# Kernel tuning notes

Hardware: AMD Instinct MI355X
Metric: run time of the kernel (lower is better)

## Reference

```python
import jax, jax.numpy as jnp
import numpy as np

Q_DIM = 9   # state(7) + action(2)
KV_DIM = 5  # fixed by get_input_tensors: 4 relative features + r_trans
H = 3
D = KV_DIM * H  # 15


def setup_inputs() -> dict:
    key = jax.random.key(0)
    ks = jax.random.split(key, 16)
    b, t = 32, 256

    def u(k, shape, fan_in):
        lim = (1.0 / fan_in) ** 0.5
        return jax.random.uniform(k, shape, jnp.float32, -lim, lim)

    return {
        "state": jax.random.normal(ks[0], (b, t, 7), jnp.float32),
        "action": jax.random.normal(ks[1], (b, t, 2), jnp.float32),
        "Wk": u(ks[2], (D, KV_DIM), KV_DIM),
        "Wq": u(ks[3], (D, Q_DIM), Q_DIM),
        "Wv": u(ks[4], (D, KV_DIM), KV_DIM),
        "att_bias": jax.random.uniform(ks[5], (KV_DIM,), jnp.float32, -0.1, 0.1),
        "Wscore": u(ks[6], (1, KV_DIM), KV_DIM),
        "bscore": u(ks[7], (1,), KV_DIM),
        "g1": jnp.ones((D,), jnp.float32),
        "beta1": jnp.zeros((D,), jnp.float32),
        "W1": u(ks[8], (5 * D, D), D),
        "bff1": u(ks[9], (5 * D,), D),
        "W2": u(ks[10], (D, 5 * D), 5 * D),
        "bff2": u(ks[11], (D,), 5 * D),
        "g2": jnp.ones((D,), jnp.float32),
        "beta2": jnp.zeros((D,), jnp.float32),
    }


def _layernorm(x, g, b, eps=1e-5):
    m = jnp.mean(x, axis=-1, keepdims=True)
    v = jnp.var(x, axis=-1, keepdims=True)
    return (x - m) * jax.lax.rsqrt(v + eps) * g + b


def _get_input_tensors(state):
    b, t, _ = state.shape
    init = state[..., :4]                                  # (b,t,4)
    rel = init[:, None, :, :] - init[:, :, None, :]        # (b,t,t,4): row i, col j -> s_j - s_i
    xy = rel.reshape(b, t, t, 2, 2).transpose(0, 1, 2, 4, 3)  # [...,0,:]=(x,vx), [...,1,:]=(y,vy)
    ang = -state[..., -1] + 0.5 * jnp.pi                   # (b,t)
    c = jnp.cos(ang)[:, None, :, None]                     # broadcast over row dim -> angle of col j
    s = jnp.sin(ang)[:, None, :, None]
    xr = xy[..., 0, :] * c - xy[..., 1, :] * s             # (b,t,t,2)
    yr = xy[..., 0, :] * s + xy[..., 1, :] * c
    rel = jnp.concatenate([xr, yr], axis=3)                # [xn,vxn,yn,vyn]
    rel = rel.reshape(b, t, t, 2, 2).transpose(0, 1, 2, 4, 3).reshape(b, t, t, 4)  # [xn,yn,vxn,vyn]
    # drop diagonal (j != i) via precomputed off-diagonal column indices
    rows = jnp.arange(t)[:, None]
    j = jnp.arange(t - 1)[None, :]
    cols = j + (j >= rows)                                 # (t,t-1)
    rel = rel[:, rows, cols, :]                            # (b,t,t-1,4)
    r = jnp.sqrt(rel[..., 0] ** 2 + rel[..., 1] ** 2)[..., None]  # (b,t,t-1,1)
    r_trans = 1.0 / (1.0 + jnp.exp(-1.0 + 5.0 * (r - 0.2)))
    kv_x = jnp.concatenate([rel[..., :2] / r, rel[..., 2:], r_trans], axis=-1)  # (b,t,t-1,5)
    return state, kv_x


def reference(state, action, Wk, Wq, Wv, att_bias, Wscore, bscore,
              g1, beta1, W1, bff1, W2, bff2, g2, beta2):
    q_x, kv_x = _get_input_tensors(state)
    q_x = jnp.concatenate([q_x, action], axis=-1)          # (b,t,Q_DIM)
    b, t, tm1, _ = kv_x.shape

    keys = (kv_x @ Wk.T).reshape(b, t, tm1, H, KV_DIM)     # (b,t,t-1,h,k)
    queries = (q_x @ Wq.T).reshape(b, t, 1, H, KV_DIM)
    e = jnp.tanh(keys + queries + att_bias)
    score = (e @ Wscore.T + bscore)[..., 0]                # (b,t,t-1,h)
    values = (kv_x @ Wv.T).reshape(b, t, tm1, H, KV_DIM)
    w = jax.nn.softmax(score, axis=2)                      # softmax over the t-1 neighbours
    x = jnp.einsum('btjh,btjhk->bthk', w, values).reshape(b, t, H * KV_DIM)

    x = _layernorm(x, g1, beta1)
    y = jax.nn.relu(x @ W1.T + bff1) @ W2.T + bff2
    x = x + y
    return _layernorm(x, g2, beta2)
```

## Files before the change

kernel.cpp:

```cpp
#include <hip/hip_runtime.h>
#include <math.h>

#define TT   256
#define TM1  255
#define QD   9
#define KD   5
#define NH   3
#define DD   15
#define HID  75
#define NR   18

#define K2E  2.8853900817779268f
#define L2E  1.4426950408889634f
#define INVK 0.34657359027997264f

__device__ __forceinline__ float fast_rcp(float x) {
    return __builtin_amdgcn_rcpf(x);
}

__device__ __forceinline__ float exp2_raw(float x) {
    float r; asm("v_exp_f32 %0, %1" : "=v"(r) : "v"(x)); return r;
}

template<int CTRL>
__device__ __forceinline__ float dpp_add(float x) {
    int y = __builtin_amdgcn_update_dpp(0, __float_as_int(x), CTRL, 0xf, 0xf, true);
    return x + __int_as_float(y);
}

__device__ __forceinline__ float wave_sum63(float x) {
    x = dpp_add<0x111>(x);
    x = dpp_add<0x112>(x);
    x = dpp_add<0x114>(x);
    x = dpp_add<0x118>(x);
    x = dpp_add<0x142>(x);
    x = dpp_add<0x143>(x);
    return x;
}

__device__ __forceinline__ float bcast(float x, int l) {
    return __int_as_float(__builtin_amdgcn_readlane(__float_as_int(x), l));
}

__global__ __launch_bounds__(256)
void fused_block_kernel(const float* __restrict__ state,
                        const float* __restrict__ action,
                        const float* __restrict__ Wk,
                        const float* __restrict__ Wq,
                        const float* __restrict__ Wv,
                        const float* __restrict__ att_bias,
                        const float* __restrict__ Wscore,
                        const float* __restrict__ bscore,
                        const float* __restrict__ g1,
                        const float* __restrict__ beta1,
                        const float* __restrict__ W1,
                        const float* __restrict__ bff1,
                        const float* __restrict__ W2,
                        const float* __restrict__ bff2,
                        const float* __restrict__ g2,
                        const float* __restrict__ beta2,
                        float* __restrict__ out)
{
    const int tid  = threadIdx.x;
    const int lane = tid & 63;
    const int wv   = __builtin_amdgcn_readfirstlane(tid >> 6);
    const int qgrp = blockIdx.x * 4 + wv;
    const int b    = qgrp >> 8;
    const int qi   = qgrp & 255;

    __shared__ float s_h[4][76];

    const float* __restrict__ sb  = state + (size_t)b*TT*7;
    const float* __restrict__ sti = sb + qi*7;

    float row[4][7];
    #pragma unroll
    for (int pp = 0; pp < 4; pp++) {
        const int mmp = lane + pp*64;
        int jj = mmp + (mmp >= qi ? 1 : 0);
        jj = (jj < TT) ? jj : (TT-1);
        const float* stj = sb + jj*7;
        #pragma unroll
        for (int k = 0; k < 7; k++) row[pp][k] = stj[k];
    }

    const float si0 = sti[0], si1 = sti[1], si2 = sti[2], si3 = sti[3];

    float qv = 0.0f;
    if (lane < DD) {
        float acc = att_bias[lane % KD];
        #pragma unroll
        for (int k = 0; k < 7; k++) acc = fmaf(Wq[lane*QD+k], sti[k], acc);
        acc = fmaf(Wq[lane*QD+7], action[((size_t)b*TT+qi)*2 + 0], acc);
        acc = fmaf(Wq[lane*QD+8], action[((size_t)b*TT+qi)*2 + 1], acc);
        qv = acc * K2E;
    }
    float qb2[DD];
    #pragma unroll
    for (int d = 0; d < DD; d++) qb2[d] = bcast(qv, d);

    float w2[KD];
    float Cn = bscore[0];
    #pragma unroll
    for (int kk = 0; kk < KD; kk++) { float w = Wscore[kk]; w2[kk] = -K2E*w; Cn += w; }
    const float C2 = L2E * Cn;

    float f0[4], f1[4], f2[4], f3[4], f4[4], Cp[4];
    #pragma unroll
    for (int pp = 0; pp < 4; pp++) {
        const float d0 = row[pp][0]-si0, d1 = row[pp][1]-si1;
        const float d2 = row[pp][2]-si2, d3 = row[pp][3]-si3;
        const float th = row[pp][6];
        const float cs = __sinf(th);
        const float sn = __cosf(th);
        const float xr0 = d0*cs - d1*sn, yr0 = d0*sn + d1*cs;
        const float xr1 = d2*cs - d3*sn, yr1 = d2*sn + d3*cs;
        const float s2   = fmaxf(fmaf(xr0, xr0, yr0*yr0), 1e-12f);
        const float rinv = __builtin_amdgcn_rsqf(s2);
        const float r    = s2 * rinv;
        const float rt   = fast_rcp(1.0f + exp2_raw(fmaf(7.213475204444817f, r,
                                                         -2.8853900817779268f)));
        const float t = K2E * rinv;
        f0[pp] = t * xr0;
        f1[pp] = t * yr0;
        f2[pp] = K2E * xr1;
        f3[pp] = K2E * yr1;
        f4[pp] = K2E * rt;
        const int mm = lane + pp*64;
        Cp[pp] = (mm < TM1) ? C2 : -100.0f;
    }

    float red[NR];
    #pragma unroll
    for (int n = 0; n < NR; n++) red[n] = 0.0f;

    #pragma unroll
    for (int pp = 0; pp < 4; pp++) {
        #pragma unroll
        for (int h = 0; h < NH; h++) {
            float sc = Cp[pp];
            #pragma unroll
            for (int kk = 0; kk < KD; kk++) {
                const int d = h*KD + kk;
                float a = qb2[d];
                a = fmaf(Wk[d*KD+0], f0[pp], a);
                a = fmaf(Wk[d*KD+1], f1[pp], a);
                a = fmaf(Wk[d*KD+2], f2[pp], a);
                a = fmaf(Wk[d*KD+3], f3[pp], a);
                a = fmaf(Wk[d*KD+4], f4[pp], a);
                sc = fmaf(w2[kk], fast_rcp(exp2_raw(a) + 1.0f), sc);
            }
            const float p = exp2_raw(sc);
            red[h] += p;
            red[NH+h*KD+0] = fmaf(p, f0[pp], red[NH+h*KD+0]);
            red[NH+h*KD+1] = fmaf(p, f1[pp], red[NH+h*KD+1]);
            red[NH+h*KD+2] = fmaf(p, f2[pp], red[NH+h*KD+2]);
            red[NH+h*KD+3] = fmaf(p, f3[pp], red[NH+h*KD+3]);
            red[NH+h*KD+4] = fmaf(p, f4[pp], red[NH+h*KD+4]);
        }
    }

    #pragma unroll
    for (int n = 0; n < NR; n++) red[n] = wave_sum63(red[n]);
    float fin[NR];
    #pragma unroll
    for (int n = 0; n < NR; n++) fin[n] = bcast(red[n], 63);

    float xm = 0.0f;
    if (lane < DD) {
        const int h = lane / KD;
        float acc = 0.0f;
        #pragma unroll
        for (int c = 0; c < KD; c++) acc = fmaf(Wv[lane*KD+c], fin[NH+h*KD+c], acc);
        xm = acc * fast_rcp(fin[h]) * INVK;
    }

    float s1 = xm, sq = xm*xm;
    #pragma unroll
    for (int off = 8; off >= 1; off >>= 1) {
        s1 += __shfl_xor(s1, off, 16);
        sq += __shfl_xor(sq, off, 16);
    }
    const float mu1   = s1 * (1.0f/DD);
    const float rstd1 = rsqrtf(sq * (1.0f/DD) - mu1*mu1 + 1e-5f);
    float xln = 0.0f;
    if (lane < DD) xln = (xm - mu1) * rstd1 * g1[lane] + beta1[lane];

    float xs[DD];
    #pragma unroll
    for (int d = 0; d < DD; d++) xs[d] = bcast(xln, d);

    {
        float h0 = bff1[lane];
        #pragma unroll
        for (int k = 0; k < DD; k++) h0 = fmaf(W1[lane*DD+k], xs[k], h0);
        s_h[wv][lane] = fmaxf(h0, 0.0f);
        if (lane < HID-64) {
            float h1 = bff1[lane+64];
            #pragma unroll
            for (int k = 0; k < DD; k++) h1 = fmaf(W1[(lane+64)*DD+k], xs[k], h1);
            s_h[wv][lane+64] = fmaxf(h1, 0.0f);
        }
    }

    const int c2  = lane >> 4;
    const int d2c = lane & 15;
    const int cc  = (c2 < 3) ? c2 : 2;
    const int dc  = (d2c < DD) ? d2c : 0;
    float acc2 = 0.0f;
    #pragma unroll
    for (int k = 0; k < 25; k++)
        acc2 = fmaf(W2[dc*HID + cc*25 + k], s_h[wv][cc*25 + k], acc2);
    acc2 = (c2 < 3) ? acc2 : 0.0f;
    acc2 += __shfl_xor(acc2, 16);
    acc2 += __shfl_xor(acc2, 32);

    float x2 = 0.0f;
    if (lane < DD) x2 = xln + bff2[lane] + acc2;
    float t1 = x2, t2 = x2*x2;
    #pragma unroll
    for (int off = 8; off >= 1; off >>= 1) {
        t1 += __shfl_xor(t1, off, 16);
        t2 += __shfl_xor(t2, off, 16);
    }
    const float mu2   = t1 * (1.0f/DD);
    const float rstd2 = rsqrtf(t2 * (1.0f/DD) - mu2*mu2 + 1e-5f);
    if (lane < DD)
        out[(size_t)qgrp*DD + lane] = (x2 - mu2) * rstd2 * g2[lane] + beta2[lane];
}

extern "C" void kernel_launch(void* const* d_in, const int* in_sizes, int n_in,
                              void* d_out, int out_size, void* d_ws, size_t ws_size,
                              hipStream_t stream) {
    const float* state    = (const float*)d_in[0];
    const float* action   = (const float*)d_in[1];
    const float* Wk       = (const float*)d_in[2];
    const float* Wq       = (const float*)d_in[3];
    const float* Wv       = (const float*)d_in[4];
    const float* att_bias = (const float*)d_in[5];
    const float* Wscore   = (const float*)d_in[6];
    const float* bscore   = (const float*)d_in[7];
    const float* g1       = (const float*)d_in[8];
    const float* beta1    = (const float*)d_in[9];
    const float* W1       = (const float*)d_in[10];
    const float* bff1     = (const float*)d_in[11];
    const float* W2       = (const float*)d_in[12];
    const float* bff2     = (const float*)d_in[13];
    const float* g2       = (const float*)d_in[14];
    const float* beta2    = (const float*)d_in[15];
    float* out = (float*)d_out;

    dim3 grid(32 * 256 / 4);
    dim3 block(256);
    fused_block_kernel<<<grid, block, 0, stream>>>(
        state, action, Wk, Wq, Wv, att_bias, Wscore, bscore,
        g1, beta1, W1, bff1, W2, bff2, g2, beta2, out);
}
```

Baseline: 26.30 us.

## Stage batch state and trig in shared memory, fuse feature and score loops

Each block now loads the batch's 256 state rows once, computes sin/cos once per row into LDS, and every wave reads its neighbour data from LDS. Previously each wave loaded all 256 rows from global memory and recomputed the trig itself. The feature computation and the attention-score loop are merged so per-neighbour features stay in scalar registers instead of 4-wide arrays. Launch bounds now request 8 blocks per CU to raise occupancy. In exchange the kernel adds a __syncthreads and about 6 KB of LDS per block, and the occupancy hint may force register spills.

```diff
diff --git a/kernel.cpp b/kernel.cpp
--- a/kernel.cpp
+++ b/kernel.cpp
@@ -42,7 +42,7 @@
     return __int_as_float(__builtin_amdgcn_readlane(__float_as_int(x), l));
 }
 
-__global__ __launch_bounds__(256)
+__global__ __launch_bounds__(256, 8)
 void fused_block_kernel(const float* __restrict__ state,
                         const float* __restrict__ action,
                         const float* __restrict__ Wk,
@@ -68,24 +68,23 @@
     const int b    = qgrp >> 8;
     const int qi   = qgrp & 255;
 
+    __shared__ float s_s0[TT], s_s1[TT], s_s2[TT], s_s3[TT], s_sn[TT], s_cs[TT];
     __shared__ float s_h[4][76];
 
-    const float* __restrict__ sb  = state + (size_t)b*TT*7;
+    const float* __restrict__ sb = state + (size_t)b*TT*7;
+
+    {
+        const float* sj = sb + tid*7;
+        const float th = sj[6];
+        s_s0[tid] = sj[0];
+        s_s1[tid] = sj[1];
+        s_s2[tid] = sj[2];
+        s_s3[tid] = sj[3];
+        s_cs[tid] = __sinf(th);
+        s_sn[tid] = __cosf(th);
+    }
+
     const float* __restrict__ sti = sb + qi*7;
-
-    float row[4][7];
-    #pragma unroll
-    for (int pp = 0; pp < 4; pp++) {
-        const int mmp = lane + pp*64;
-        int jj = mmp + (mmp >= qi ? 1 : 0);
-        jj = (jj < TT) ? jj : (TT-1);
-        const float* stj = sb + jj*7;
-        #pragma unroll
-        for (int k = 0; k < 7; k++) row[pp][k] = stj[k];
-    }
-
-    const float si0 = sti[0], si1 = sti[1], si2 = sti[2], si3 = sti[3];
-
     float qv = 0.0f;
     if (lane < DD) {
         float acc = att_bias[lane % KD];
@@ -105,14 +104,24 @@
     for (int kk = 0; kk < KD; kk++) { float w = Wscore[kk]; w2[kk] = -K2E*w; Cn += w; }
     const float C2 = L2E * Cn;
 
-    float f0[4], f1[4], f2[4], f3[4], f4[4], Cp[4];
+    const float si0 = sti[0], si1 = sti[1], si2 = sti[2], si3 = sti[3];
+
+    __syncthreads();
+
+    float red[NR];
+    #pragma unroll
+    for (int n = 0; n < NR; n++) red[n] = 0.0f;
+
     #pragma unroll
     for (int pp = 0; pp < 4; pp++) {
-        const float d0 = row[pp][0]-si0, d1 = row[pp][1]-si1;
-        const float d2 = row[pp][2]-si2, d3 = row[pp][3]-si3;
-        const float th = row[pp][6];
-        const float cs = __sinf(th);
-        const float sn = __cosf(th);
+        const int mm = lane + pp*64;
+        int jj = mm + (mm >= qi ? 1 : 0);
+        jj = (jj < TT) ? jj : (TT-1);
+        const float Cp = (mm < TM1) ? C2 : -100.0f;
+
+        const float d0 = s_s0[jj]-si0, d1 = s_s1[jj]-si1;
+        const float d2 = s_s2[jj]-si2, d3 = s_s3[jj]-si3;
+        const float cs = s_cs[jj],     sn = s_sn[jj];
         const float xr0 = d0*cs - d1*sn, yr0 = d0*sn + d1*cs;
         const float xr1 = d2*cs - d3*sn, yr1 = d2*sn + d3*cs;
         const float s2   = fmaxf(fmaf(xr0, xr0, yr0*yr0), 1e-12f);
@@ -120,43 +129,34 @@
         const float r    = s2 * rinv;
         const float rt   = fast_rcp(1.0f + exp2_raw(fmaf(7.213475204444817f, r,
                                                          -2.8853900817779268f)));
-        const float t = K2E * rinv;
-        f0[pp] = t * xr0;
-        f1[pp] = t * yr0;
-        f2[pp] = K2E * xr1;
-        f3[pp] = K2E * yr1;
-        f4[pp] = K2E * rt;
-        const int mm = lane + pp*64;
-        Cp[pp] = (mm < TM1) ? C2 : -100.0f;
-    }
-
-    float red[NR];
-    #pragma unroll
-    for (int n = 0; n < NR; n++) red[n] = 0.0f;
-
-    #pragma unroll
-    for (int pp = 0; pp < 4; pp++) {
+        const float t  = K2E * rinv;
+        const float f0 = t * xr0;
+        const float f1 = t * yr0;
+        const float f2 = K2E * xr1;
+        const float f3 = K2E * yr1;
+        const float f4 = K2E * rt;
+
         #pragma unroll
         for (int h = 0; h < NH; h++) {
-            float sc = Cp[pp];
+            float sc = Cp;
             #pragma unroll
             for (int kk = 0; kk < KD; kk++) {
                 const int d = h*KD + kk;
                 float a = qb2[d];
-                a = fmaf(Wk[d*KD+0], f0[pp], a);
-                a = fmaf(Wk[d*KD+1], f1[pp], a);
-                a = fmaf(Wk[d*KD+2], f2[pp], a);
-                a = fmaf(Wk[d*KD+3], f3[pp], a);
-                a = fmaf(Wk[d*KD+4], f4[pp], a);
+                a = fmaf(Wk[d*KD+0], f0, a);
+                a = fmaf(Wk[d*KD+1], f1, a);
+                a = fmaf(Wk[d*KD+2], f2, a);
+                a = fmaf(Wk[d*KD+3], f3, a);
+                a = fmaf(Wk[d*KD+4], f4, a);
                 sc = fmaf(w2[kk], fast_rcp(exp2_raw(a) + 1.0f), sc);
             }
             const float p = exp2_raw(sc);
             red[h] += p;
-            red[NH+h*KD+0] = fmaf(p, f0[pp], red[NH+h*KD+0]);
-            red[NH+h*KD+1] = fmaf(p, f1[pp], red[NH+h*KD+1]);
-            red[NH+h*KD+2] = fmaf(p, f2[pp], red[NH+h*KD+2]);
-            red[NH+h*KD+3] = fmaf(p, f3[pp], red[NH+h*KD+3]);
-            red[NH+h*KD+4] = fmaf(p, f4[pp], red[NH+h*KD+4]);
+            red[NH+h*KD+0] = fmaf(p, f0, red[NH+h*KD+0]);
+            red[NH+h*KD+1] = fmaf(p, f1, red[NH+h*KD+1]);
+            red[NH+h*KD+2] = fmaf(p, f2, red[NH+h*KD+2]);
+            red[NH+h*KD+3] = fmaf(p, f3, red[NH+h*KD+3]);
+            red[NH+h*KD+4] = fmaf(p, f4, red[NH+h*KD+4]);
         }
     }
 
```

Result: slower. 30.67 us (+16.6%).
